# Kernel tuning notes

Measured on AMD Instinct MI355X. Metric: run time of the kernel, lower is better.

Reference implementation:

```python
import jax, jax.numpy as jnp
import numpy as np

N = 50000      # nodes
E = 600000     # edges
IN = 128       # input_dim
HID = 128      # hidden_dim
OUT = 128      # output_dim
H = 4          # heads
D = OUT // H   # head dim
R = 4          # rel_num
L = 2          # n_layer
M = 10000      # len(idx)
EPS = 1e-5


def setup_inputs() -> dict:
    key = jax.random.key(0)
    ks = jax.random.split(key, 16)
    f = jax.random.normal
    inp = {
        "x": f(ks[0], (N, IN), jnp.float32),
        "proj_w": f(ks[1], (IN, HID), jnp.float32) / np.sqrt(IN).astype(np.float32),
        "proj_b": jnp.zeros((HID,), jnp.float32),
        "bn_gamma": jnp.ones((HID,), jnp.float32),
        "bn_beta": jnp.zeros((HID,), jnp.float32),
        # per-layer HGTConv params (stacked on leading L axis; layer0 in=HID, layer1 in=OUT, equal here)
        "q_w": f(ks[2], (L, HID, OUT), jnp.float32) / np.sqrt(HID).astype(np.float32),
        "q_b": jnp.zeros((L, OUT), jnp.float32),
        "k_w": f(ks[3], (L, HID, OUT), jnp.float32) / np.sqrt(HID).astype(np.float32),
        "k_b": jnp.zeros((L, OUT), jnp.float32),
        "v_w": f(ks[4], (L, HID, OUT), jnp.float32) / np.sqrt(HID).astype(np.float32),
        "v_b": jnp.zeros((L, OUT), jnp.float32),
        "a_w": f(ks[5], (L, OUT, OUT), jnp.float32) / np.sqrt(OUT).astype(np.float32),
        "a_b": jnp.zeros((L, OUT), jnp.float32),
        "skip": jnp.ones((L,), jnp.float32),
        "a_rel": f(ks[6], (L, R, H, D, D), jnp.float32) / np.sqrt(D).astype(np.float32),
        "m_rel": f(ks[7], (L, R, H, D, D), jnp.float32) / np.sqrt(D).astype(np.float32),
        "p_rel": jnp.ones((L, R, H), jnp.float32),
        "edge_index": jax.random.randint(ks[8], (2, E), 0, N, dtype=jnp.int32),
        "edge_type": jax.random.randint(ks[9], (E,), 0, R, dtype=jnp.int32),
        "idx": jax.random.randint(ks[10], (M,), 0, N, dtype=jnp.int32),
    }
    return inp


def _hgt_forward(x, proj_w, proj_b, bn_gamma, bn_beta, q_w, q_b, k_w, k_b, v_w, v_b,
                 a_w, a_b, skip, a_rel, m_rel, p_rel, edge_index, edge_type, idx):
    # proj + BatchNorm1d (training-mode batch statistics, biased variance)
    h = x @ proj_w + proj_b
    mu = h.mean(axis=0)
    var = jnp.mean((h - mu) ** 2, axis=0)
    h = (h - mu) * jax.lax.rsqrt(var + EPS) * bn_gamma + bn_beta

    src, dst = edge_index[0], edge_index[1]          # message from src(j) to dst(i)
    seg = dst * R + edge_type                        # per-(dst, relation) softmax segments
    scale = np.float32(1.0 / np.sqrt(D))

    for l in range(L):
        q = (h @ q_w[l] + q_b[l]).reshape(N, H, D)
        k = (h @ k_w[l] + k_b[l]).reshape(N, H, D)
        v = (h @ v_w[l] + v_b[l]).reshape(N, H, D)
        # relation-specific key/value transforms for every node/relation: [N,R,H,D]
        k_all = jnp.einsum('nhd,rhde->nrhe', k, a_rel[l])
        v_all = jnp.einsum('nhd,rhde->nrhe', v, m_rel[l])
        k_e = k_all[src, edge_type]                  # [E,H,D]
        v_e = v_all[src, edge_type]                  # [E,H,D]
        score = jnp.sum(q[dst] * k_e, axis=-1) * p_rel[l][edge_type] * scale  # [E,H]
        # per-relation segment softmax over incoming edges of each dst node
        smax = jax.ops.segment_max(score, seg, num_segments=N * R)
        e = jnp.exp(score - smax[seg])
        denom = jax.ops.segment_sum(e, seg, num_segments=N * R)
        alpha = e / denom[seg]                        # [E,H]
        out = jax.ops.segment_sum(alpha[..., None] * v_e, dst, num_segments=N)
        out = out.reshape(N, OUT)
        out = jax.nn.gelu(out, approximate=False) @ a_w[l] + a_b[l]
        b = jax.nn.sigmoid(skip[l])                   # learned skip gate
        h = b * out + (1.0 - b) * h                   # dims match -> residual mix
    return h[idx]


def reference(x, proj_w, proj_b, bn_gamma, bn_beta, q_w, q_b, k_w, k_b, v_w, v_b,
              a_w, a_b, skip, a_rel, m_rel, p_rel, edge_index, edge_type, idx):
    return _hgt_forward(x, proj_w, proj_b, bn_gamma, bn_beta, q_w, q_b, k_w, k_b,
                        v_w, v_b, a_w, a_b, skip, a_rel, m_rel, p_rel,
                        edge_index, edge_type, idx)
```

## Files before the change

### kernel.cpp

```cpp
#include <hip/hip_runtime.h>
#include <math.h>

#define NN 50000
#define EE 600000
#define MOUT 10000
#define DEGCAP 384
#define NT4 (NN * 4)

typedef short bf16x8 __attribute__((ext_vector_type(8)));
typedef float f32x4 __attribute__((ext_vector_type(4)));

__device__ __forceinline__ unsigned short f2bf(float x) {
    unsigned int u = __float_as_uint(x);
    u = (u + 0x7FFFu + ((u >> 16) & 1u)) >> 16;
    return (unsigned short)u;
}
__device__ __forceinline__ float bf2f(unsigned int b) {
    return __uint_as_float(b << 16);
}

__global__ __launch_bounds__(256) void prep_kernel(
    const float* __restrict__ proj_w, const float* __restrict__ a_w,
    const float* __restrict__ q_w, const float* __restrict__ q_b,
    const float* __restrict__ a_rel,
    const float* __restrict__ k_w, const float* __restrict__ k_b,
    const float* __restrict__ v_w, const float* __restrict__ v_b,
    const float* __restrict__ m_rel, const float* __restrict__ p_rel,
    const float* __restrict__ x,
    unsigned short* __restrict__ wt_pa, unsigned short* __restrict__ qkvw,
    float* __restrict__ fbias, unsigned short* __restrict__ msg_wt,
    unsigned short* __restrict__ x_bf, int* __restrict__ cnt,
    float* __restrict__ stats)
{
    const int b = blockIdx.x, t = threadIdx.x;
    if (b < 192) {
        int wi = b >> 6;
        int flat = (b & 63) * 256 + t;
        int n = flat >> 7, c = flat & 127;
        const float* src = (wi == 0) ? proj_w : (wi == 1) ? a_w : a_w + 16384;
        wt_pa[(size_t)wi * 16384 + n * 128 + c] = f2bf(src[c * 128 + n]);
    } else if (b < 960) {
        int q = b - 192;
        int l = q >= 384 ? 1 : 0;
        int flat = (q - l * 384) * 256 + t;
        int nrow = flat >> 7, c = flat & 127;
        unsigned short* wt = qkvw + (size_t)l * 98304;
        float* fb = fbias + l * 768;
        if (nrow < 512) {
            int r = nrow >> 7, hh = (nrow >> 5) & 3, d = nrow & 31;
            float prl = p_rel[l * 16 + r * 4 + hh] * 0.17677669529663687f;
            const float* qwc = q_w + (size_t)l * 16384 + c * 128 + hh * 32;
            const float* ar  = a_rel + (size_t)(l * 4 + r) * 4096 + hh * 1024 + d * 32;
            float s = 0.f;
            #pragma unroll 8
            for (int e = 0; e < 32; ++e) s += qwc[e] * ar[e];
            wt[(size_t)nrow * 128 + c] = f2bf(s * prl);
            if (c == 0) {
                const float* qb = q_b + l * 128 + hh * 32;
                float bb = 0.f;
                #pragma unroll 8
                for (int e = 0; e < 32; ++e) bb += qb[e] * ar[e];
                fb[nrow] = bb * prl;
            }
        } else {
            int j = nrow - 512;
            int tt = j >> 2, s = j & 3;
            int col = 2 * tt + (s & 1);
            const float* w  = (s < 2) ? k_w : v_w;
            const float* bb = (s < 2) ? k_b : v_b;
            wt[(size_t)nrow * 128 + c] = f2bf(w[(size_t)l * 16384 + c * 128 + col]);
            if (c == 0) fb[nrow] = bb[l * 128 + col];
        }
    } else if (b < 1472) {
        int q = b - 960;
        int l = q >= 256 ? 1 : 0;
        int flat = (q - l * 256) * 256 + t;
        int n = flat >> 9, kk = flat & 511;
        int h = n >> 5, e = n & 31;
        int r = kk >> 7, h2 = (kk >> 5) & 3, d = kk & 31;
        float val = (h2 == h) ? m_rel[(size_t)(l * 4 + r) * 4096 + h * 1024 + d * 32 + e] : 0.f;
        msg_wt[(size_t)l * 65536 + (size_t)n * 512 + kk] = f2bf(val);
    } else if (b < 7722) {
        int i = (b - 1472) * 256 + t;
        if (i < NN * 32) {
            float4 v = ((const float4*)x)[i];
            uint2 pk;
            pk.x = (unsigned int)f2bf(v.x) | ((unsigned int)f2bf(v.y) << 16);
            pk.y = (unsigned int)f2bf(v.z) | ((unsigned int)f2bf(v.w) << 16);
            ((uint2*)x_bf)[i] = pk;
        }
    } else {
        int i = (b - 7722) * 256 + t;
        if (i < NT4) cnt[i] = 0;
        if (i < 256) stats[i] = 0.f;
    }
}

__global__ __launch_bounds__(256) void hist_kernel(const int* __restrict__ ei,
    const int* __restrict__ et, int* __restrict__ cnt, int E)
{
    int e = blockIdx.x * 256 + threadIdx.x;
    if (e < E) atomicAdd(&cnt[ei[E + e] * 4 + et[e]], 1);
}

__global__ __launch_bounds__(256) void scan_block_kernel(const int* __restrict__ cnt,
    int* __restrict__ excl, int* __restrict__ bsum, int n)
{
    __shared__ int tmp[256];
    int i = blockIdx.x * 256 + threadIdx.x;
    int v = (i < n) ? cnt[i] : 0;
    tmp[threadIdx.x] = v;
    __syncthreads();
    for (int ofs = 1; ofs < 256; ofs <<= 1) {
        int t = (threadIdx.x >= ofs) ? tmp[threadIdx.x - ofs] : 0;
        __syncthreads();
        tmp[threadIdx.x] += t;
        __syncthreads();
    }
    if (i < n) excl[i] = tmp[threadIdx.x] - v;
    if (threadIdx.x == 255) bsum[blockIdx.x] = tmp[255];
}

__global__ __launch_bounds__(256) void scan_add_kernel(int* __restrict__ excl,
    const int* __restrict__ bsum, int* __restrict__ fill, int n, int total)
{
    __shared__ int red[256];
    const int b = blockIdx.x;
    int partial = 0;
    for (int j = threadIdx.x; j < b; j += 256) partial += bsum[j];
    red[threadIdx.x] = partial;
    __syncthreads();
    for (int ofs = 128; ofs > 0; ofs >>= 1) {
        if (threadIdx.x < ofs) red[threadIdx.x] += red[threadIdx.x + ofs];
        __syncthreads();
    }
    int prefix = red[0];
    int i = b * 256 + threadIdx.x;
    if (i < n) {
        int o = excl[i] + prefix;
        excl[i] = o;
        fill[i] = o;
    }
    if (b == 0 && threadIdx.x == 0) excl[n] = total;
}

__global__ __launch_bounds__(256) void scatter_kernel(const int* __restrict__ ei,
    const int* __restrict__ et, int* __restrict__ fill, int* __restrict__ pack, int E)
{
    int e = blockIdx.x * 256 + threadIdx.x;
    if (e >= E) return;
    int seg = ei[E + e] * 4 + et[e];
    int p = atomicAdd(&fill[seg], 1);
    pack[p] = ei[e];
}

__global__ __launch_bounds__(256) void projstats_kernel(
    const unsigned short* __restrict__ A, const unsigned short* __restrict__ Wt,
    const float* __restrict__ bias, unsigned short* __restrict__ Cb,
    float* __restrict__ stats, int M)
{
    __shared__ unsigned short As[128 * 40];
    __shared__ unsigned short Bs[128 * 40];
    const int t = threadIdx.x;
    const int wave = t >> 6, lane = t & 63;
    const int quad = lane >> 4, l16 = lane & 15;
    const int row0 = blockIdx.x * 128;
    const int wr = (wave & 1) * 64, wc = (wave >> 1) * 64;
    const int sr = t >> 1, sc = (t & 1) * 16;
    const int grow = row0 + sr;

    f32x4 acc[4][4];
    #pragma unroll
    for (int i = 0; i < 4; ++i)
        #pragma unroll
        for (int j = 0; j < 4; ++j)
            acc[i][j] = (f32x4){0.f, 0.f, 0.f, 0.f};

    uint4 av0 = make_uint4(0,0,0,0), av1 = av0, bv0, bv1;
    if (grow < M) {
        const uint4* ap = (const uint4*)(A + (size_t)grow * 128 + sc);
        av0 = ap[0]; av1 = ap[1];
    }
    {
        const uint4* bp = (const uint4*)(Wt + (size_t)sr * 128 + sc);
        bv0 = bp[0]; bv1 = bp[1];
    }
    for (int it = 0; it < 4; ++it) {
        __syncthreads();
        *(uint4*)(As + sr * 40 + sc)     = av0;
        *(uint4*)(As + sr * 40 + sc + 8) = av1;
        *(uint4*)(Bs + sr * 40 + sc)     = bv0;
        *(uint4*)(Bs + sr * 40 + sc + 8) = bv1;
        __syncthreads();
        if (it + 1 < 4) {
            int kb = (it + 1) * 32;
            if (grow < M) {
                const uint4* ap = (const uint4*)(A + (size_t)grow * 128 + kb + sc);
                av0 = ap[0]; av1 = ap[1];
            }
            const uint4* bp = (const uint4*)(Wt + (size_t)sr * 128 + kb + sc);
            bv0 = bp[0]; bv1 = bp[1];
        }
        bf16x8 af[4], bfr[4];
        #pragma unroll
        for (int f = 0; f < 4; ++f) {
            af[f]  = *(const bf16x8*)(As + (wr + f * 16 + l16) * 40 + quad * 8);
            bfr[f] = *(const bf16x8*)(Bs + (wc + f * 16 + l16) * 40 + quad * 8);
        }
        #pragma unroll
        for (int fr = 0; fr < 4; ++fr)
            #pragma unroll
            for (int fc = 0; fc < 4; ++fc)
                acc[fr][fc] = __builtin_amdgcn_mfma_f32_16x16x32_bf16(
                    af[fr], bfr[fc], acc[fr][fc], 0, 0, 0);
    }

    #pragma unroll
    for (int fc = 0; fc < 4; ++fc) {
        const int col = wc + fc * 16 + l16;
        const float bv = bias[col];
        float s = 0.f, s2 = 0.f;
        #pragma unroll
        for (int fr = 0; fr < 4; ++fr)
            #pragma unroll
            for (int reg = 0; reg < 4; ++reg) {
                int row = row0 + wr + fr * 16 + quad * 4 + reg;
                float val = acc[fr][fc][reg] + bv;
                if (row < M) {
                    Cb[(size_t)row * 128 + col] = f2bf(val);
                    s += val; s2 += val * val;
                }
            }
        s  += __shfl_xor(s, 16);  s  += __shfl_xor(s, 32);
        s2 += __shfl_xor(s2, 16); s2 += __shfl_xor(s2, 32);
        if (quad == 0) {
            atomicAdd(&stats[col], s);
            atomicAdd(&stats[128 + col], s2);
        }
    }
}

__global__ __launch_bounds__(256) void bnqkv_kernel(
    const unsigned short* __restrict__ hb, const float* __restrict__ stats,
    const float* __restrict__ gamma, const float* __restrict__ beta,
    const unsigned short* __restrict__ qkvw, const float* __restrict__ fbias,
    unsigned short* __restrict__ hn, unsigned short* __restrict__ qkv, int M)
{
    __shared__ unsigned short hS[128 * 136];
    __shared__ unsigned short Bs[128 * 40];
    __shared__ float mulS[128], addS[128];
    const int t = threadIdx.x;
    const int row0 = blockIdx.x * 128;
    if (t < 128) {
        float invN = 1.f / 50000.f;
        float mu = stats[t] * invN;
        float var = stats[128 + t] * invN - mu * mu;
        float ml = rsqrtf(var + 1e-5f) * gamma[t];
        mulS[t] = ml;
        addS[t] = beta[t] - mu * ml;
    }
    __syncthreads();
    #pragma unroll
    for (int u = 0; u < 8; ++u) {
        int li = t + u * 256;
        int row = li >> 4, c0 = (li & 15) * 8;
        uint4 pk = make_uint4(0, 0, 0, 0);
        if (row0 + row < M)
            pk = ((const uint4*)(hb + (size_t)(row0 + row) * 128))[li & 15];
        unsigned int w[4] = {pk.x, pk.y, pk.z, pk.w};
        uint4 o;
        unsigned int ov[4];
        #pragma unroll
        for (int g = 0; g < 4; ++g) {
            int c = c0 + g * 2;
            float a0 = bf2f(w[g] & 0xFFFFu) * mulS[c]     + addS[c];
            float a1 = bf2f(w[g] >> 16)     * mulS[c + 1] + addS[c + 1];
            ov[g] = (unsigned int)f2bf(a0) | ((unsigned int)f2bf(a1) << 16);
        }
        o.x = ov[0]; o.y = ov[1]; o.z = ov[2]; o.w = ov[3];
        *(uint4*)(hS + row * 136 + c0) = o;
        if (row0 + row < M)
            ((uint4*)(hn + (size_t)(row0 + row) * 128))[li & 15] = o;
    }
    __syncthreads();

    const int wave = t >> 6, lane = t & 63;
    const int quad = lane >> 4, l16 = lane & 15;
    const int wr = (wave & 1) * 64, wcl = (wave >> 1) * 64;
    const int sr = t >> 1, scc = (t & 1) * 16;
    for (int ch = 0; ch < 6; ++ch) {
        f32x4 acc[4][4];
        #pragma unroll
        for (int i = 0; i < 4; ++i)
            #pragma unroll
            for (int j = 0; j < 4; ++j)
                acc[i][j] = (f32x4){0.f, 0.f, 0.f, 0.f};
        for (int it = 0; it < 4; ++it) {
            __syncthreads();
            const uint4* bp = (const uint4*)(qkvw + (size_t)(ch * 128 + sr) * 128 + it * 32 + scc);
            *(uint4*)(Bs + sr * 40 + scc)     = bp[0];
            *(uint4*)(Bs + sr * 40 + scc + 8) = bp[1];
            __syncthreads();
            bf16x8 af[4], bfr[4];
            #pragma unroll
            for (int f = 0; f < 4; ++f) {
                af[f]  = *(const bf16x8*)(hS + (wr + f * 16 + l16) * 136 + it * 32 + quad * 8);
                bfr[f] = *(const bf16x8*)(Bs + (wcl + f * 16 + l16) * 40 + quad * 8);
            }
            #pragma unroll
            for (int fr = 0; fr < 4; ++fr)
                #pragma unroll
                for (int fc = 0; fc < 4; ++fc)
                    acc[fr][fc] = __builtin_amdgcn_mfma_f32_16x16x32_bf16(
                        af[fr], bfr[fc], acc[fr][fc], 0, 0, 0);
        }
        float b4[4];
        #pragma unroll
        for (int fc = 0; fc < 4; ++fc)
            b4[fc] = fbias[ch * 128 + wcl + fc * 16 + l16];
        #pragma unroll
        for (int fr = 0; fr < 4; ++fr)
            #pragma unroll
            for (int reg = 0; reg < 4; ++reg) {
                int row = row0 + wr + fr * 16 + quad * 4 + reg;
                if (row >= M) continue;
                #pragma unroll
                for (int fc = 0; fc < 4; ++fc) {
                    int col = ch * 128 + wcl + fc * 16 + l16;
                    qkv[(size_t)row * 768 + col] = f2bf(acc[fr][fc][reg] + b4[fc]);
                }
            }
    }
}

__global__ __launch_bounds__(256) void agg_fused_kernel(
    const unsigned short* __restrict__ qkv,
    const int* __restrict__ off4, const int* __restrict__ pack,
    const int* __restrict__ rowmap, unsigned short* __restrict__ aggb, int count)
{
    __shared__ int spack[4][DEGCAP];
    const int wv = threadIdx.x >> 6;
    const int lane = threadIdx.x & 63;
    const int unit = blockIdx.x * 4 + wv;
    if (unit >= count) return;
    const int node = rowmap ? __builtin_amdgcn_readfirstlane(rowmap[unit]) : unit;

    int off_r[5];
    #pragma unroll
    for (int i = 0; i < 5; ++i)
        off_r[i] = __builtin_amdgcn_readfirstlane(off4[node * 4 + i]);
    const int beg = off_r[0];
    const int deg = off_r[4] - beg;
    const bool cached = deg <= DEGCAP;

    const unsigned int* qrow = (const unsigned int*)(qkv + (size_t)node * 768);

    if (cached) {
        for (int i = lane; i < deg; i += 64) spack[wv][i] = pack[beg + i];
        asm volatile("s_waitcnt vmcnt(0) lgkmcnt(0)" ::: "memory");
    }

    unsigned int outw[4];
    for (int r = 0; r < 4; ++r) {
        unsigned int qu = qrow[r * 64 + lane];
        float qx = bf2f(qu & 0xFFFFu);
        float qy = bf2f(qu >> 16);
        float den = 0.f, ax = 0.f, ay = 0.f;

        if (cached) {
            const int rb = off_r[r] - beg, re = off_r[r + 1] - beg;
            for (int i = rb; i < re; i += 4) {
                unsigned int ku[4], vu[4];
                #pragma unroll
                for (int j = 0; j < 4; ++j) {
                    int ii = i + j; if (ii >= re) ii = re - 1;
                    int src = spack[wv][ii];
                    uint2 kv = *(const uint2*)(qkv + (size_t)src * 768 + 512 + lane * 4);
                    ku[j] = kv.x; vu[j] = kv.y;
                }
                float p[4];
                #pragma unroll
                for (int j = 0; j < 4; ++j)
                    p[j] = qx * bf2f(ku[j] & 0xFFFFu) + qy * bf2f(ku[j] >> 16);
                #pragma unroll
                for (int j = 0; j < 4; ++j) {
                    p[j] += __shfl_xor(p[j], 1); p[j] += __shfl_xor(p[j], 2);
                    p[j] += __shfl_xor(p[j], 4); p[j] += __shfl_xor(p[j], 8);
                }
                #pragma unroll
                for (int j = 0; j < 4; ++j) {
                    float s = fminf(fmaxf(p[j], -80.f), 80.f);
                    float e = __expf(s);
                    if (i + j >= re) e = 0.f;
                    den += e;
                    ax += e * bf2f(vu[j] & 0xFFFFu);
                    ay += e * bf2f(vu[j] >> 16);
                }
            }
        } else {
            for (int pp = off_r[r]; pp < off_r[r + 1]; ++pp) {
                int src = __builtin_amdgcn_readfirstlane(pack[pp]);
                uint2 kv = *(const uint2*)(qkv + (size_t)src * 768 + 512 + lane * 4);
                float p0 = qx * bf2f(kv.x & 0xFFFFu) + qy * bf2f(kv.x >> 16);
                p0 += __shfl_xor(p0, 1); p0 += __shfl_xor(p0, 2);
                p0 += __shfl_xor(p0, 4); p0 += __shfl_xor(p0, 8);
                float e = __expf(fminf(fmaxf(p0, -80.f), 80.f));
                den += e;
                ax += e * bf2f(kv.y & 0xFFFFu);
                ay += e * bf2f(kv.y >> 16);
            }
        }
        float inv = den > 0.f ? 1.f / den : 0.f;
        outw[r] = (unsigned int)f2bf(ax * inv) | ((unsigned int)f2bf(ay * inv) << 16);
    }
    unsigned int* op = (unsigned int*)(aggb + (size_t)unit * 512);
    #pragma unroll
    for (int r = 0; r < 4; ++r) op[r * 64 + lane] = outw[r];
}

__global__ __launch_bounds__(256) void mlpqkv_kernel(
    const unsigned short* __restrict__ A, const unsigned short* __restrict__ W3t,
    const unsigned short* __restrict__ AWt, const float* __restrict__ a_bias,
    const float* __restrict__ skipv, const unsigned short* __restrict__ hres,
    const unsigned short* __restrict__ qkvw1, const float* __restrict__ fbias1,
    unsigned short* __restrict__ h1, unsigned short* __restrict__ qkv, int M)
{
    __shared__ unsigned short As[128 * 40];
    __shared__ unsigned short Bs[128 * 40];
    __shared__ unsigned short msgS[128 * 136];
    const int t = threadIdx.x;
    const int wave = t >> 6, lane = t & 63;
    const int quad = lane >> 4, l16 = lane & 15;
    const int row0 = blockIdx.x * 128;
    const int wr = (wave & 1) * 64, wcl = (wave >> 1) * 64;
    const int sr = t >> 1, scc = (t & 1) * 16;
    const int grow = row0 + sr;
    const bool rvalid = grow < M;

    f32x4 acc[4][4];
    #pragma unroll
    for (int i = 0; i < 4; ++i)
        #pragma unroll
        for (int j = 0; j < 4; ++j)
            acc[i][j] = (f32x4){0.f, 0.f, 0.f, 0.f};

    uint4 av0 = make_uint4(0,0,0,0), av1 = av0, bv0, bv1;
    if (rvalid) {
        const uint4* ap = (const uint4*)(A + (size_t)grow * 512 + scc);
        av0 = ap[0]; av1 = ap[1];
    }
    {
        const uint4* bp = (const uint4*)(W3t + (size_t)sr * 512 + scc);
        bv0 = bp[0]; bv1 = bp[1];
    }
    for (int it = 0; it < 16; ++it) {
        __syncthreads();
        *(uint4*)(As + sr * 40 + scc)     = av0;
        *(uint4*)(As + sr * 40 + scc + 8) = av1;
        *(uint4*)(Bs + sr * 40 + scc)     = bv0;
        *(uint4*)(Bs + sr * 40 + scc + 8) = bv1;
        __syncthreads();
        if (it + 1 < 16) {
            int kb = (it + 1) * 32;
            if (rvalid) {
                const uint4* ap = (const uint4*)(A + (size_t)grow * 512 + kb + scc);
                av0 = ap[0]; av1 = ap[1];
            }
            const uint4* bp = (const uint4*)(W3t + (size_t)sr * 512 + kb + scc);
            bv0 = bp[0]; bv1 = bp[1];
        }
        bf16x8 af[4], bfr[4];
        #pragma unroll
        for (int f = 0; f < 4; ++f) {
            af[f]  = *(const bf16x8*)(As + (wr + f * 16 + l16) * 40 + quad * 8);
            bfr[f] = *(const bf16x8*)(Bs + (wcl + f * 16 + l16) * 40 + quad * 8);
        }
        #pragma unroll
        for (int fr = 0; fr < 4; ++fr)
            #pragma unroll
            for (int fc = 0; fc < 4; ++fc)
                acc[fr][fc] = __builtin_amdgcn_mfma_f32_16x16x32_bf16(
                    af[fr], bfr[fc], acc[fr][fc], 0, 0, 0);
    }

    #pragma unroll
    for (int fr = 0; fr < 4; ++fr)
        #pragma unroll
        for (int reg = 0; reg < 4; ++reg) {
            int rl = wr + fr * 16 + quad * 4 + reg;
            #pragma unroll
            for (int fc = 0; fc < 4; ++fc) {
                int col = wcl + fc * 16 + l16;
                float v = acc[fr][fc][reg];
                float gl = 0.5f * v * (1.f + erff(v * 0.70710678118654752f));
                msgS[rl * 136 + col] = f2bf(gl);
            }
        }

    f32x4 acc2[4][4];
    #pragma unroll
    for (int i = 0; i < 4; ++i)
        #pragma unroll
        for (int j = 0; j < 4; ++j)
            acc2[i][j] = (f32x4){0.f, 0.f, 0.f, 0.f};
    for (int it = 0; it < 4; ++it) {
        __syncthreads();
        const uint4* bp = (const uint4*)(AWt + (size_t)sr * 128 + it * 32 + scc);
        *(uint4*)(Bs + sr * 40 + scc)     = bp[0];
        *(uint4*)(Bs + sr * 40 + scc + 8) = bp[1];
        __syncthreads();
        bf16x8 af[4], bfr[4];
        #pragma unroll
        for (int f = 0; f < 4; ++f) {
            af[f]  = *(const bf16x8*)(msgS + (wr + f * 16 + l16) * 136 + it * 32 + quad * 8);
            bfr[f] = *(const bf16x8*)(Bs + (wcl + f * 16 + l16) * 40 + quad * 8);
        }
        #pragma unroll
        for (int fr = 0; fr < 4; ++fr)
            #pragma unroll
            for (int fc = 0; fc < 4; ++fc)
                acc2[fr][fc] = __builtin_amdgcn_mfma_f32_16x16x32_bf16(
                    af[fr], bfr[fc], acc2[fr][fc], 0, 0, 0);
    }

    const float gate = 1.f / (1.f + __expf(-skipv[0]));
    __syncthreads();
    #pragma unroll
    for (int fr = 0; fr < 4; ++fr)
        #pragma unroll
        for (int reg = 0; reg < 4; ++reg) {
            int rl = wr + fr * 16 + quad * 4 + reg;
            int row = row0 + rl;
            #pragma unroll
            for (int fc = 0; fc < 4; ++fc) {
                int col = wcl + fc * 16 + l16;
                float val = acc2[fr][fc][reg] + a_bias[col];
                float nv = val;
                if (row < M) {
                    unsigned int hu = hres[(size_t)row * 128 + col];
                    nv = gate * val + (1.f - gate) * bf2f(hu);
                    h1[(size_t)row * 128 + col] = f2bf(nv);
                }
                msgS[rl * 136 + col] = f2bf(nv);
            }
        }

    for (int ch = 0; ch < 6; ++ch) {
        f32x4 acc3[4][4];
        #pragma unroll
        for (int i = 0; i < 4; ++i)
            #pragma unroll
            for (int j = 0; j < 4; ++j)
                acc3[i][j] = (f32x4){0.f, 0.f, 0.f, 0.f};
        for (int it = 0; it < 4; ++it) {
            __syncthreads();
            const uint4* bp = (const uint4*)(qkvw1 + (size_t)(ch * 128 + sr) * 128 + it * 32 + scc);
            *(uint4*)(Bs + sr * 40 + scc)     = bp[0];
            *(uint4*)(Bs + sr * 40 + scc + 8) = bp[1];
            __syncthreads();
            bf16x8 af[4], bfr[4];
            #pragma unroll
            for (int f = 0; f < 4; ++f) {
                af[f]  = *(const bf16x8*)(msgS + (wr + f * 16 + l16) * 136 + it * 32 + quad * 8);
                bfr[f] = *(const bf16x8*)(Bs + (wcl + f * 16 + l16) * 40 + quad * 8);
            }
            #pragma unroll
            for (int fr = 0; fr < 4; ++fr)
                #pragma unroll
                for (int fc = 0; fc < 4; ++fc)
                    acc3[fr][fc] = __builtin_amdgcn_mfma_f32_16x16x32_bf16(
                        af[fr], bfr[fc], acc3[fr][fc], 0, 0, 0);
        }
        float b4[4];
        #pragma unroll
        for (int fc = 0; fc < 4; ++fc)
            b4[fc] = fbias1[ch * 128 + wcl + fc * 16 + l16];
        #pragma unroll
        for (int fr = 0; fr < 4; ++fr)
            #pragma unroll
            for (int reg = 0; reg < 4; ++reg) {
                int row = row0 + wr + fr * 16 + quad * 4 + reg;
                if (row >= M) continue;
                #pragma unroll
                for (int fc = 0; fc < 4; ++fc) {
                    int col = ch * 128 + wcl + fc * 16 + l16;
                    qkv[(size_t)row * 768 + col] = f2bf(acc3[fr][fc][reg] + b4[fc]);
                }
            }
    }
}

__global__ __launch_bounds__(256) void mlp1_kernel(
    const unsigned short* __restrict__ A, const unsigned short* __restrict__ W3t,
    const unsigned short* __restrict__ AWt, const float* __restrict__ a_bias,
    const float* __restrict__ skipv, const unsigned short* __restrict__ hres,
    const int* __restrict__ rowmap, float* __restrict__ out, int M)
{
    __shared__ unsigned short As[128 * 40];
    __shared__ unsigned short Bs[128 * 40];
    __shared__ unsigned short msgS[128 * 136];
    const int t = threadIdx.x;
    const int wave = t >> 6, lane = t & 63;
    const int quad = lane >> 4, l16 = lane & 15;
    const int row0 = blockIdx.x * 128;
    const int wr = (wave & 1) * 64, wcl = (wave >> 1) * 64;
    const int sr = t >> 1, scc = (t & 1) * 16;
    const int grow = row0 + sr;
    const bool rvalid = grow < M;

    f32x4 acc[4][4];
    #pragma unroll
    for (int i = 0; i < 4; ++i)
        #pragma unroll
        for (int j = 0; j < 4; ++j)
            acc[i][j] = (f32x4){0.f, 0.f, 0.f, 0.f};

    uint4 av0 = make_uint4(0,0,0,0), av1 = av0, bv0, bv1;
    if (rvalid) {
        const uint4* ap = (const uint4*)(A + (size_t)grow * 512 + scc);
        av0 = ap[0]; av1 = ap[1];
    }
    {
        const uint4* bp = (const uint4*)(W3t + (size_t)sr * 512 + scc);
        bv0 = bp[0]; bv1 = bp[1];
    }
    for (int it = 0; it < 16; ++it) {
        __syncthreads();
        *(uint4*)(As + sr * 40 + scc)     = av0;
        *(uint4*)(As + sr * 40 + scc + 8) = av1;
        *(uint4*)(Bs + sr * 40 + scc)     = bv0;
        *(uint4*)(Bs + sr * 40 + scc + 8) = bv1;
        __syncthreads();
        if (it + 1 < 16) {
            int kb = (it + 1) * 32;
            if (rvalid) {
                const uint4* ap = (const uint4*)(A + (size_t)grow * 512 + kb + scc);
                av0 = ap[0]; av1 = ap[1];
            }
            const uint4* bp = (const uint4*)(W3t + (size_t)sr * 512 + kb + scc);
            bv0 = bp[0]; bv1 = bp[1];
        }
        bf16x8 af[4], bfr[4];
        #pragma unroll
        for (int f = 0; f < 4; ++f) {
            af[f]  = *(const bf16x8*)(As + (wr + f * 16 + l16) * 40 + quad * 8);
            bfr[f] = *(const bf16x8*)(Bs + (wcl + f * 16 + l16) * 40 + quad * 8);
        }
        #pragma unroll
        for (int fr = 0; fr < 4; ++fr)
            #pragma unroll
            for (int fc = 0; fc < 4; ++fc)
                acc[fr][fc] = __builtin_amdgcn_mfma_f32_16x16x32_bf16(
                    af[fr], bfr[fc], acc[fr][fc], 0, 0, 0);
    }

    #pragma unroll
    for (int fr = 0; fr < 4; ++fr)
        #pragma unroll
        for (int reg = 0; reg < 4; ++reg) {
            int rl = wr + fr * 16 + quad * 4 + reg;
            #pragma unroll
            for (int fc = 0; fc < 4; ++fc) {
                int col = wcl + fc * 16 + l16;
                float v = acc[fr][fc][reg];
                float gl = 0.5f * v * (1.f + erff(v * 0.70710678118654752f));
                msgS[rl * 136 + col] = f2bf(gl);
            }
        }

    f32x4 acc2[4][4];
    #pragma unroll
    for (int i = 0; i < 4; ++i)
        #pragma unroll
        for (int j = 0; j < 4; ++j)
            acc2[i][j] = (f32x4){0.f, 0.f, 0.f, 0.f};
    for (int it = 0; it < 4; ++it) {
        __syncthreads();
        const uint4* bp = (const uint4*)(AWt + (size_t)sr * 128 + it * 32 + scc);
        *(uint4*)(Bs + sr * 40 + scc)     = bp[0];
        *(uint4*)(Bs + sr * 40 + scc + 8) = bp[1];
        __syncthreads();
        bf16x8 af[4], bfr[4];
        #pragma unroll
        for (int f = 0; f < 4; ++f) {
            af[f]  = *(const bf16x8*)(msgS + (wr + f * 16 + l16) * 136 + it * 32 + quad * 8);
            bfr[f] = *(const bf16x8*)(Bs + (wcl + f * 16 + l16) * 40 + quad * 8);
        }
        #pragma unroll
        for (int fr = 0; fr < 4; ++fr)
            #pragma unroll
            for (int fc = 0; fc < 4; ++fc)
                acc2[fr][fc] = __builtin_amdgcn_mfma_f32_16x16x32_bf16(
                    af[fr], bfr[fc], acc2[fr][fc], 0, 0, 0);
    }

    const float gate = 1.f / (1.f + __expf(-skipv[0]));
    #pragma unroll
    for (int fr = 0; fr < 4; ++fr)
        #pragma unroll
        for (int reg = 0; reg < 4; ++reg) {
            int row = row0 + wr + fr * 16 + quad * 4 + reg;
            if (row >= M) continue;
            int hrow = rowmap[row];
            #pragma unroll
            for (int fc = 0; fc < 4; ++fc) {
                int col = wcl + fc * 16 + l16;
                float val = acc2[fr][fc][reg] + a_bias[col];
                float nv = gate * val + (1.f - gate) * bf2f((unsigned int)hres[(size_t)hrow * 128 + col]);
                out[(size_t)row * 128 + col] = nv;
            }
        }
}

extern "C" void kernel_launch(void* const* d_in, const int* in_sizes, int n_in,
                              void* d_out, int out_size, void* d_ws, size_t ws_size,
                              hipStream_t stream)
{
    const float* x      = (const float*)d_in[0];
    const float* proj_w = (const float*)d_in[1];
    const float* proj_b = (const float*)d_in[2];
    const float* bn_g   = (const float*)d_in[3];
    const float* bn_b   = (const float*)d_in[4];
    const float* q_w    = (const float*)d_in[5];
    const float* q_b    = (const float*)d_in[6];
    const float* k_w    = (const float*)d_in[7];
    const float* k_b    = (const float*)d_in[8];
    const float* v_w    = (const float*)d_in[9];
    const float* v_b    = (const float*)d_in[10];
    const float* a_w    = (const float*)d_in[11];
    const float* a_b    = (const float*)d_in[12];
    const float* skip   = (const float*)d_in[13];
    const float* a_rel  = (const float*)d_in[14];
    const float* m_rel  = (const float*)d_in[15];
    const float* p_rel  = (const float*)d_in[16];
    const int* edge_index = (const int*)d_in[17];
    const int* edge_type  = (const int*)d_in[18];
    const int* idx        = (const int*)d_in[19];
    float* out = (float*)d_out;

    const int N = NN, E = EE;
    float* ws = (float*)d_ws;
    size_t o = 0;
    float* stats  = ws + o;  o += 256;
    float* fbias  = ws + o;  o += 2 * 768;
    int* cnt  = (int*)(ws + o); o += NT4;
    int* off4 = (int*)(ws + o); o += NT4 + 1;
    int* fill = (int*)(ws + o); o += NT4;
    int* bsum = (int*)(ws + o); o += 1024;
    int* pack = (int*)(ws + o); o += E;
    unsigned short* x_bf   = (unsigned short*)(ws + o); o += (size_t)N * 64;
    unsigned short* h_bf   = (unsigned short*)(ws + o); o += (size_t)N * 64;
    unsigned short* hn_bf  = (unsigned short*)(ws + o); o += (size_t)N * 64;
    unsigned short* h1_bf  = (unsigned short*)(ws + o); o += (size_t)N * 64;
    unsigned short* qkv_bf = (unsigned short*)(ws + o); o += (size_t)N * 384;
    unsigned short* agg_bf = (unsigned short*)(ws + o); o += (size_t)N * 256;
    unsigned short* wt_pa  = (unsigned short*)(ws + o); o += 3 * 16384 / 2;
    unsigned short* qkvw   = (unsigned short*)(ws + o); o += 2 * 98304 / 2;
    unsigned short* msg_wt = (unsigned short*)(ws + o); o += 2 * 65536 / 2;

    const int NB4 = (NT4 + 255) / 256;
    const int g = (N + 127) / 128;

    prep_kernel<<<7722 + NB4, 256, 0, stream>>>(
        proj_w, a_w, q_w, q_b, a_rel, k_w, k_b, v_w, v_b, m_rel, p_rel, x,
        wt_pa, qkvw, fbias, msg_wt, x_bf, cnt, stats);

    hist_kernel<<<(E + 255) / 256, 256, 0, stream>>>(edge_index, edge_type, cnt, E);
    scan_block_kernel<<<NB4, 256, 0, stream>>>(cnt, off4, bsum, NT4);
    scan_add_kernel<<<NB4, 256, 0, stream>>>(off4, bsum, fill, NT4, E);
    scatter_kernel<<<(E + 255) / 256, 256, 0, stream>>>(edge_index, edge_type, fill, pack, E);

    projstats_kernel<<<g, 256, 0, stream>>>(x_bf, wt_pa, proj_b, h_bf, stats, N);

    bnqkv_kernel<<<g, 256, 0, stream>>>(h_bf, stats, bn_g, bn_b, qkvw, fbias,
                                        hn_bf, qkv_bf, N);

    agg_fused_kernel<<<(N + 3) / 4, 256, 0, stream>>>(qkv_bf, off4, pack, nullptr,
                                                      agg_bf, N);

    mlpqkv_kernel<<<g, 256, 0, stream>>>(agg_bf, msg_wt, wt_pa + 16384, a_b, skip,
                                         hn_bf, qkvw + 98304, fbias + 768,
                                         h1_bf, qkv_bf, N);

    agg_fused_kernel<<<(MOUT + 3) / 4, 256, 0, stream>>>(qkv_bf, off4, pack, idx,
                                                         agg_bf, MOUT);

    mlp1_kernel<<<(MOUT + 127) / 128, 256, 0, stream>>>(agg_bf, msg_wt + 65536,
                                                        wt_pa + 2 * 16384, a_b + 128,
                                                        skip + 1, h1_bf, idx, out, MOUT);
}
```

Measured before the change: 441.9 us.

## Load GEMM operands directly from global memory, drop LDS staging and barriers

Result: slower. 579.3 us (+31.1%).

```diff
diff --git a/kernel.cpp b/kernel.cpp
--- a/kernel.cpp
+++ b/kernel.cpp
@@ -6,6 +6,7 @@
 #define MOUT 10000
 #define DEGCAP 384
 #define NT4 (NN * 4)
+#define MS 168
 
 typedef short bf16x8 __attribute__((ext_vector_type(8)));
 typedef float f32x4 __attribute__((ext_vector_type(4)));
@@ -240,14 +241,13 @@
     }
 }
 
-__global__ __launch_bounds__(256) void bnqkv_kernel(
+__global__ __launch_bounds__(256, 3) void bnqkv_kernel(
     const unsigned short* __restrict__ hb, const float* __restrict__ stats,
     const float* __restrict__ gamma, const float* __restrict__ beta,
     const unsigned short* __restrict__ qkvw, const float* __restrict__ fbias,
     unsigned short* __restrict__ hn, unsigned short* __restrict__ qkv, int M)
 {
-    __shared__ unsigned short hS[128 * 136];
-    __shared__ unsigned short Bs[128 * 40];
+    __shared__ unsigned short hS[128 * MS];
     __shared__ float mulS[128], addS[128];
     const int t = threadIdx.x;
     const int row0 = blockIdx.x * 128;
@@ -278,7 +278,7 @@
             ov[g] = (unsigned int)f2bf(a0) | ((unsigned int)f2bf(a1) << 16);
         }
         o.x = ov[0]; o.y = ov[1]; o.z = ov[2]; o.w = ov[3];
-        *(uint4*)(hS + row * 136 + c0) = o;
+        *(uint4*)(hS + row * MS + c0) = o;
         if (row0 + row < M)
             ((uint4*)(hn + (size_t)(row0 + row) * 128))[li & 15] = o;
     }
@@ -287,7 +287,6 @@
     const int wave = t >> 6, lane = t & 63;
     const int quad = lane >> 4, l16 = lane & 15;
     const int wr = (wave & 1) * 64, wcl = (wave >> 1) * 64;
-    const int sr = t >> 1, scc = (t & 1) * 16;
     for (int ch = 0; ch < 6; ++ch) {
         f32x4 acc[4][4];
         #pragma unroll
@@ -295,17 +294,14 @@
             #pragma unroll
             for (int j = 0; j < 4; ++j)
                 acc[i][j] = (f32x4){0.f, 0.f, 0.f, 0.f};
+        #pragma unroll
         for (int it = 0; it < 4; ++it) {
-            __syncthreads();
-            const uint4* bp = (const uint4*)(qkvw + (size_t)(ch * 128 + sr) * 128 + it * 32 + scc);
-            *(uint4*)(Bs + sr * 40 + scc)     = bp[0];
-            *(uint4*)(Bs + sr * 40 + scc + 8) = bp[1];
-            __syncthreads();
             bf16x8 af[4], bfr[4];
             #pragma unroll
             for (int f = 0; f < 4; ++f) {
-                af[f]  = *(const bf16x8*)(hS + (wr + f * 16 + l16) * 136 + it * 32 + quad * 8);
-                bfr[f] = *(const bf16x8*)(Bs + (wcl + f * 16 + l16) * 40 + quad * 8);
+                af[f]  = *(const bf16x8*)(hS + (wr + f * 16 + l16) * MS + it * 32 + quad * 8);
+                bfr[f] = *(const bf16x8*)(qkvw + (size_t)(ch * 128 + wcl + f * 16 + l16) * 128
+                                          + it * 32 + quad * 8);
             }
             #pragma unroll
             for (int fr = 0; fr < 4; ++fr)
@@ -418,24 +414,26 @@
     for (int r = 0; r < 4; ++r) op[r * 64 + lane] = outw[r];
 }
 
-__global__ __launch_bounds__(256) void mlpqkv_kernel(
+__global__ __launch_bounds__(256, 3) void mlpqkv_kernel(
     const unsigned short* __restrict__ A, const unsigned short* __restrict__ W3t,
     const unsigned short* __restrict__ AWt, const float* __restrict__ a_bias,
     const float* __restrict__ skipv, const unsigned short* __restrict__ hres,
     const unsigned short* __restrict__ qkvw1, const float* __restrict__ fbias1,
     unsigned short* __restrict__ h1, unsigned short* __restrict__ qkv, int M)
 {
-    __shared__ unsigned short As[128 * 40];
-    __shared__ unsigned short Bs[128 * 40];
-    __shared__ unsigned short msgS[128 * 136];
+    __shared__ unsigned short msgS[128 * MS];
     const int t = threadIdx.x;
     const int wave = t >> 6, lane = t & 63;
     const int quad = lane >> 4, l16 = lane & 15;
     const int row0 = blockIdx.x * 128;
     const int wr = (wave & 1) * 64, wcl = (wave >> 1) * 64;
-    const int sr = t >> 1, scc = (t & 1) * 16;
-    const int grow = row0 + sr;
-    const bool rvalid = grow < M;
+
+    size_t arow[4];
+    #pragma unroll
+    for (int f = 0; f < 4; ++f) {
+        int r = row0 + wr + f * 16 + l16;
+        arow[f] = (size_t)(r < M ? r : M - 1) * 512;
+    }
 
     f32x4 acc[4][4];
     #pragma unroll
@@ -443,37 +441,13 @@
         #pragma unroll
         for (int j = 0; j < 4; ++j)
             acc[i][j] = (f32x4){0.f, 0.f, 0.f, 0.f};
-
-    uint4 av0 = make_uint4(0,0,0,0), av1 = av0, bv0, bv1;
-    if (rvalid) {
-        const uint4* ap = (const uint4*)(A + (size_t)grow * 512 + scc);
-        av0 = ap[0]; av1 = ap[1];
-    }
-    {
-        const uint4* bp = (const uint4*)(W3t + (size_t)sr * 512 + scc);
-        bv0 = bp[0]; bv1 = bp[1];
-    }
     for (int it = 0; it < 16; ++it) {
-        __syncthreads();
-        *(uint4*)(As + sr * 40 + scc)     = av0;
-        *(uint4*)(As + sr * 40 + scc + 8) = av1;
-        *(uint4*)(Bs + sr * 40 + scc)     = bv0;
-        *(uint4*)(Bs + sr * 40 + scc + 8) = bv1;
-        __syncthreads();
-        if (it + 1 < 16) {
-            int kb = (it + 1) * 32;
-            if (rvalid) {
-                const uint4* ap = (const uint4*)(A + (size_t)grow * 512 + kb + scc);
-                av0 = ap[0]; av1 = ap[1];
-            }
-            const uint4* bp = (const uint4*)(W3t + (size_t)sr * 512 + kb + scc);
-            bv0 = bp[0]; bv1 = bp[1];
-        }
         bf16x8 af[4], bfr[4];
         #pragma unroll
         for (int f = 0; f < 4; ++f) {
-            af[f]  = *(const bf16x8*)(As + (wr + f * 16 + l16) * 40 + quad * 8);
-            bfr[f] = *(const bf16x8*)(Bs + (wcl + f * 16 + l16) * 40 + quad * 8);
+            af[f]  = *(const bf16x8*)(A + arow[f] + it * 32 + quad * 8);
+            bfr[f] = *(const bf16x8*)(W3t + (size_t)(wcl + f * 16 + l16) * 512
+                                      + it * 32 + quad * 8);
         }
         #pragma unroll
         for (int fr = 0; fr < 4; ++fr)
@@ -493,9 +467,10 @@
                 int col = wcl + fc * 16 + l16;
                 float v = acc[fr][fc][reg];
                 float gl = 0.5f * v * (1.f + erff(v * 0.70710678118654752f));
-                msgS[rl * 136 + col] = f2bf(gl);
-            }
-        }
+                msgS[rl * MS + col] = f2bf(gl);
+            }
+        }
+    __syncthreads();
 
     f32x4 acc2[4][4];
     #pragma unroll
@@ -503,17 +478,14 @@
         #pragma unroll
         for (int j = 0; j < 4; ++j)
             acc2[i][j] = (f32x4){0.f, 0.f, 0.f, 0.f};
+    #pragma unroll
     for (int it = 0; it < 4; ++it) {
-        __syncthreads();
-        const uint4* bp = (const uint4*)(AWt + (size_t)sr * 128 + it * 32 + scc);
-        *(uint4*)(Bs + sr * 40 + scc)     = bp[0];
-        *(uint4*)(Bs + sr * 40 + scc + 8) = bp[1];
-        __syncthreads();
         bf16x8 af[4], bfr[4];
         #pragma unroll
         for (int f = 0; f < 4; ++f) {
-            af[f]  = *(const bf16x8*)(msgS + (wr + f * 16 + l16) * 136 + it * 32 + quad * 8);
-            bfr[f] = *(const bf16x8*)(Bs + (wcl + f * 16 + l16) * 40 + quad * 8);
+            af[f]  = *(const bf16x8*)(msgS + (wr + f * 16 + l16) * MS + it * 32 + quad * 8);
+            bfr[f] = *(const bf16x8*)(AWt + (size_t)(wcl + f * 16 + l16) * 128
+                                      + it * 32 + quad * 8);
         }
         #pragma unroll
         for (int fr = 0; fr < 4; ++fr)
@@ -541,9 +513,10 @@
                     nv = gate * val + (1.f - gate) * bf2f(hu);
                     h1[(size_t)row * 128 + col] = f2bf(nv);
                 }
-                msgS[rl * 136 + col] = f2bf(nv);
-            }
-        }
+                msgS[rl * MS + col] = f2bf(nv);
+            }
+        }
+    __syncthreads();
 
     for (int ch = 0; ch < 6; ++ch) {
         f32x4 acc3[4][4];
@@ -552,17 +525,14 @@
             #pragma unroll
             for (int j = 0; j < 4; ++j)
                 acc3[i][j] = (f32x4){0.f, 0.f, 0.f, 0.f};
+        #pragma unroll
         for (int it = 0; it < 4; ++it) {
-            __syncthreads();
-            const uint4* bp = (const uint4*)(qkvw1 + (size_t)(ch * 128 + sr) * 128 + it * 32 + scc);
-            *(uint4*)(Bs + sr * 40 + scc)     = bp[0];
-            *(uint4*)(Bs + sr * 40 + scc + 8) = bp[1];
-            __syncthreads();
             bf16x8 af[4], bfr[4];
             #pragma unroll
             for (int f = 0; f < 4; ++f) {
-                af[f]  = *(const bf16x8*)(msgS + (wr + f * 16 + l16) * 136 + it * 32 + quad * 8);
-                bfr[f] = *(const bf16x8*)(Bs + (wcl + f * 16 + l16) * 40 + quad * 8);
+                af[f]  = *(const bf16x8*)(msgS + (wr + f * 16 + l16) * MS + it * 32 + quad * 8);
+                bfr[f] = *(const bf16x8*)(qkvw1 + (size_t)(ch * 128 + wcl + f * 16 + l16) * 128
+                                          + it * 32 + quad * 8);
             }
             #pragma unroll
             for (int fr = 0; fr < 4; ++fr)
@@ -590,23 +560,25 @@
     }
 }
 
-__global__ __launch_bounds__(256) void mlp1_kernel(
+__global__ __launch_bounds__(256, 3) void mlp1_kernel(
     const unsigned short* __restrict__ A, const unsigned short* __restrict__ W3t,
     const unsigned short* __restrict__ AWt, const float* __restrict__ a_bias,
     const float* __restrict__ skipv, const unsigned short* __restrict__ hres,
     const int* __restrict__ rowmap, float* __restrict__ out, int M)
 {
-    __shared__ unsigned short As[128 * 40];
-    __shared__ unsigned short Bs[128 * 40];
-    __shared__ unsigned short msgS[128 * 136];
+    __shared__ unsigned short msgS[128 * MS];
     const int t = threadIdx.x;
     const int wave = t >> 6, lane = t & 63;
     const int quad = lane >> 4, l16 = lane & 15;
     const int row0 = blockIdx.x * 128;
     const int wr = (wave & 1) * 64, wcl = (wave >> 1) * 64;
-    const int sr = t >> 1, scc = (t & 1) * 16;
-    const int grow = row0 + sr;
-    const bool rvalid = grow < M;
+
+    size_t arow[4];
+    #pragma unroll
+    for (int f = 0; f < 4; ++f) {
+        int r = row0 + wr + f * 16 + l16;
+        arow[f] = (size_t)(r < M ? r : M - 1) * 512;
+    }
 
     f32x4 acc[4][4];
     #pragma unroll
@@ -614,37 +586,13 @@
         #pragma unroll
         for (int j = 0; j < 4; ++j)
             acc[i][j] = (f32x4){0.f, 0.f, 0.f, 0.f};
-
-    uint4 av0 = make_uint4(0,0,0,0), av1 = av0, bv0, bv1;
-    if (rvalid) {
-        const uint4* ap = (const uint4*)(A + (size_t)grow * 512 + scc);
-        av0 = ap[0]; av1 = ap[1];
-    }
-    {
-        const uint4* bp = (const uint4*)(W3t + (size_t)sr * 512 + scc);
-        bv0 = bp[0]; bv1 = bp[1];
-    }
     for (int it = 0; it < 16; ++it) {
-        __syncthreads();
-        *(uint4*)(As + sr * 40 + scc)     = av0;
-        *(uint4*)(As + sr * 40 + scc + 8) = av1;
-        *(uint4*)(Bs + sr * 40 + scc)     = bv0;
-        *(uint4*)(Bs + sr * 40 + scc + 8) = bv1;
-        __syncthreads();
-        if (it + 1 < 16) {
-            int kb = (it + 1) * 32;
-            if (rvalid) {
-                const uint4* ap = (const uint4*)(A + (size_t)grow * 512 + kb + scc);
-                av0 = ap[0]; av1 = ap[1];
-            }
-            const uint4* bp = (const uint4*)(W3t + (size_t)sr * 512 + kb + scc);
-            bv0 = bp[0]; bv1 = bp[1];
-        }
         bf16x8 af[4], bfr[4];
         #pragma unroll
         for (int f = 0; f < 4; ++f) {
-            af[f]  = *(const bf16x8*)(As + (wr + f * 16 + l16) * 40 + quad * 8);
-            bfr[f] = *(const bf16x8*)(Bs + (wcl + f * 16 + l16) * 40 + quad * 8);
+            af[f]  = *(const bf16x8*)(A + arow[f] + it * 32 + quad * 8);
+            bfr[f] = *(const bf16x8*)(W3t + (size_t)(wcl + f * 16 + l16) * 512
+                                      + it * 32 + quad * 8);
         }
         #pragma unroll
         for (int fr = 0; fr < 4; ++fr)
@@ -664,9 +612,10 @@
                 int col = wcl + fc * 16 + l16;
                 float v = acc[fr][fc][reg];
                 float gl = 0.5f * v * (1.f + erff(v * 0.70710678118654752f));
-                msgS[rl * 136 + col] = f2bf(gl);
-            }
-        }
+                msgS[rl * MS + col] = f2bf(gl);
+            }
+        }
+    __syncthreads();
 
     f32x4 acc2[4][4];
     #pragma unroll
@@ -674,17 +623,14 @@
         #pragma unroll
         for (int j = 0; j < 4; ++j)
             acc2[i][j] = (f32x4){0.f, 0.f, 0.f, 0.f};
+    #pragma unroll
     for (int it = 0; it < 4; ++it) {
-        __syncthreads();
-        const uint4* bp = (const uint4*)(AWt + (size_t)sr * 128 + it * 32 + scc);
-        *(uint4*)(Bs + sr * 40 + scc)     = bp[0];
-        *(uint4*)(Bs + sr * 40 + scc + 8) = bp[1];
-        __syncthreads();
         bf16x8 af[4], bfr[4];
         #pragma unroll
         for (int f = 0; f < 4; ++f) {
-            af[f]  = *(const bf16x8*)(msgS + (wr + f * 16 + l16) * 136 + it * 32 + quad * 8);
-            bfr[f] = *(const bf16x8*)(Bs + (wcl + f * 16 + l16) * 40 + quad * 8);
+            af[f]  = *(const bf16x8*)(msgS + (wr + f * 16 + l16) * MS + it * 32 + quad * 8);
+            bfr[f] = *(const bf16x8*)(AWt + (size_t)(wcl + f * 16 + l16) * 128
+                                      + it * 32 + quad * 8);
         }
         #pragma unroll
         for (int fr = 0; fr < 4; ++fr)
```
